# Optimization experiments

Hardware: AMD Instinct MI355X
Metric: run time of the kernel (lower is better)

Reference implementation:

```python
import jax, jax.numpy as jnp
import numpy as np

D = 128      # d_model
H = 8        # heads
HD = D // H  # head dim
FF = 1024    # feedforward
L = 6        # encoder layers
LN_EPS = 1e-5


def setup_inputs() -> dict:
    key = jax.random.key(0)
    ks = jax.random.split(key, 10)
    S, B = 512, 64
    p = lambda k, shape: jax.random.normal(k, shape, dtype=jnp.float32) * 0.02
    return {
        "src": jax.random.normal(ks[0], (S, B, D), dtype=jnp.float32),
        "Wqkv": p(ks[1], (L, 3 * D, D)), "bqkv": p(ks[2], (L, 3 * D)),
        "Wo": p(ks[3], (L, D, D)), "bo": p(ks[4], (L, D)),
        "ln1_g": jnp.ones((L, D), jnp.float32), "ln1_b": jnp.zeros((L, D), jnp.float32),
        "W1": p(ks[5], (L, FF, D)), "b1": p(ks[6], (L, FF)),
        "W2": p(ks[7], (L, D, FF)), "b2": p(ks[8], (L, D)),
        "ln2_g": jnp.ones((L, D), jnp.float32), "ln2_b": jnp.zeros((L, D), jnp.float32),
    }


def _layer_norm(x, g, b):
    mu = jnp.mean(x, axis=-1, keepdims=True)
    var = jnp.mean(jnp.square(x - mu), axis=-1, keepdims=True)
    return (x - mu) * jax.lax.rsqrt(var + LN_EPS) * g + b


def _pairwise_cos(x):
    # x: (B, S, D) -> clamped cosine similarity (B, S, S); single batched GEMM
    n = jnp.linalg.norm(x, axis=-1)                      # (B, S)
    sim = jnp.einsum('bid,bjd->bij', x, x) / (n[:, :, None] * n[:, None, :])
    return jnp.maximum(sim, 1e-6)


def _encoder_layer(x, Wqkv, bqkv, Wo, bo, g1, b1ln, W1, b1, W2, b2, g2, b2ln):
    # x: (B, S, D); PyTorch post-norm TransformerEncoderLayer (ReLU), eval mode (no dropout)
    B, S, _ = x.shape
    qkv = x @ Wqkv.T + bqkv                              # (B, S, 3D)
    q, k, v = jnp.split(qkv, 3, axis=-1)
    q = q.reshape(B, S, H, HD)
    k = k.reshape(B, S, H, HD)
    v = v.reshape(B, S, H, HD)
    scores = jnp.einsum('bqhd,bkhd->bhqk', q, k) / np.float32(np.sqrt(HD))
    attn = jax.nn.softmax(scores, axis=-1)
    o = jnp.einsum('bhqk,bkhd->bqhd', attn, v).reshape(B, S, D)
    o = o @ Wo.T + bo
    x = _layer_norm(x + o, g1, b1ln)
    ff = jax.nn.relu(x @ W1.T + b1) @ W2.T + b2
    return _layer_norm(x + ff, g2, b2ln)


def reference(src, Wqkv, bqkv, Wo, bo, ln1_g, ln1_b, W1, b1, W2, b2, ln2_g, ln2_b):
    x_bsd = jnp.transpose(src, (1, 0, 2))                # (B, S, D)
    cs = _pairwise_cos(x_bsd)
    h = x_bsd
    for i in range(L):
        h = _encoder_layer(h, Wqkv[i], bqkv[i], Wo[i], bo[i], ln1_g[i], ln1_b[i],
                           W1[i], b1[i], W2[i], b2[i], ln2_g[i], ln2_b[i])
    mask = jax.nn.sigmoid(h)
    out = mask * x_bsd
    out = out / jnp.maximum(jnp.linalg.norm(out, axis=-1, keepdims=True), 1e-12)
    sim = _pairwise_cos(out) + cs
    return jnp.clip(sim * 0.5, 0.1, 0.9)
```

## Files before the change

kernel.cpp:

```cpp
#include <hip/hip_runtime.h>
#include <cstdint>
#include <cstddef>

#define SS 512
#define BB 64
#define DD 128
#define HH 8
#define HDIM 16
#define FFD 1024
#define NL 6

typedef short bf16x8 __attribute__((ext_vector_type(8)));
typedef float f32x4 __attribute__((ext_vector_type(4)));

__device__ inline uint32_t pack2(float a, float b) {
  uint32_t r;
  asm("v_cvt_pk_bf16_f32 %0, %1, %2" : "=v"(r) : "v"(a), "v"(b));
  return r;
}

#define QSCALE 0.36067376022224085f

__global__ __launch_bounds__(256) void cvt_kernel(const float* __restrict__ s,
                                                  short* __restrict__ d, int n2) {
  int i = blockIdx.x * 256 + threadIdx.x;
  if (i < n2) {
    float2 v = ((const float2*)s)[i];
    ((uint32_t*)d)[i] = pack2(v.x, v.y);
  }
}

__global__ __launch_bounds__(256) void cvt_qkv_kernel(const float* __restrict__ s,
                                                      short* __restrict__ d) {
  int i = blockIdx.x * 256 + threadIdx.x;
  if (i < NL * 384 * 64) {
    const int within = i % (384 * 64);
    const float sc = (within < 128 * 64) ? QSCALE : 1.0f;
    float2 v = ((const float2*)s)[i];
    ((uint32_t*)d)[i] = pack2(v.x * sc, v.y * sc);
  }
}

__global__ __launch_bounds__(256) void scale_bq_kernel(const float* __restrict__ s,
                                                       float* __restrict__ d) {
  int i = blockIdx.x * 256 + threadIdx.x;
  if (i < NL * 384) {
    const float sc = ((i % 384) < 128) ? QSCALE : 1.0f;
    d[i] = s[i] * sc;
  }
}

__global__ __launch_bounds__(256) void transpose_rn_kernel(const float* __restrict__ src,
                                                           float* __restrict__ x0,
                                                           float* __restrict__ h,
                                                           short* __restrict__ hb,
                                                           short* __restrict__ xn) {
  const int wave = threadIdx.x >> 6;
  const int lane = threadIdx.x & 63;
  const int row = blockIdx.x * 4 + wave;
  const int b = row >> 9;
  const int s = row & 511;
  const float2 v = ((const float2*)(src + ((size_t)s * BB + b) * DD))[lane];
  ((float2*)(x0 + (size_t)row * DD))[lane] = v;
  ((float2*)(h + (size_t)row * DD))[lane] = v;
  ((uint32_t*)hb)[(size_t)row * 64 + lane] = pack2(v.x, v.y);
  float ss = v.x * v.x + v.y * v.y;
  #pragma unroll
  for (int off = 1; off < 64; off <<= 1) ss += __shfl_xor(ss, off);
  const float r = rsqrtf(ss);
  ((uint32_t*)xn)[(size_t)row * 64 + lane] = pack2(v.x * r, v.y * r);
}

template <int MODE, bool CBF, bool RELU, bool QPERM>
__global__ __launch_bounds__(256) void mgemm(const short* __restrict__ Ab0,
                                             const short* __restrict__ Bw,
                                             const float* __restrict__ bias,
                                             void* __restrict__ Cp,
                                             int M, int N, int K,
                                             long sA, long sB, long sC) {
  __shared__ uint32_t Xs[128 * 32];
  __shared__ uint32_t Wls[128 * 32];
  const int t = threadIdx.x;
  const int wave = t >> 6, lane = t & 63;
  const int g = lane >> 4, p = lane & 15;
  const int wr = wave >> 1, wc = wave & 1;
  const int m0 = blockIdx.y * 128, n0 = blockIdx.x * 128;
  const int z = blockIdx.z;
  const short* Ab = Ab0 + (size_t)z * sA;
  const short* Bb = Bw + (size_t)z * sB;
  float* Cf = (float*)Cp + (CBF ? (size_t)0 : (size_t)z * sC);
  short* Cb = (short*)Cp;

  f32x4 acc[4][4];
  #pragma unroll
  for (int i = 0; i < 4; ++i)
    #pragma unroll
    for (int j = 0; j < 4; ++j) acc[i][j] = (f32x4){0.f, 0.f, 0.f, 0.f};

  for (int kt = 0; kt < K; kt += 64) {
    __syncthreads();
    #pragma unroll
    for (int i = 0; i < 4; ++i) {
      const int idx = t + i * 256;
      const int row = idx >> 3, kc = idx & 7;
      const uint4 w = *(const uint4*)(Ab + (size_t)(m0 + row) * K + kt + kc * 8);
      *(uint4*)(Xs + row * 32 + ((kc ^ (row & 7)) << 2)) = w;
      const uint4 u = *(const uint4*)(Bb + (size_t)(n0 + row) * K + kt + kc * 8);
      *(uint4*)(Wls + row * 32 + ((kc ^ (row & 7)) << 2)) = u;
    }
    __syncthreads();
    #pragma unroll
    for (int kc32 = 0; kc32 < 2; ++kc32) {
      bf16x8 xf[4], wf[4];
      #pragma unroll
      for (int mi = 0; mi < 4; ++mi) {
        const int row = wr * 64 + mi * 16 + p;
        union { bf16x8 v; uint4 w; } u;
        u.w = *(const uint4*)(Xs + row * 32 + (((kc32 * 4 + g) ^ (row & 7)) << 2));
        xf[mi] = u.v;
      }
      #pragma unroll
      for (int ni = 0; ni < 4; ++ni) {
        const int row = wc * 64 + ni * 16 + p;
        union { bf16x8 v; uint4 w; } u;
        u.w = *(const uint4*)(Wls + row * 32 + (((kc32 * 4 + g) ^ (row & 7)) << 2));
        wf[ni] = u.v;
      }
      #pragma unroll
      for (int mi = 0; mi < 4; ++mi)
        #pragma unroll
        for (int ni = 0; ni < 4; ++ni)
          acc[mi][ni] = __builtin_amdgcn_mfma_f32_16x16x32_bf16(wf[ni], xf[mi], acc[mi][ni], 0, 0, 0);
    }
  }

  #pragma unroll
  for (int mi = 0; mi < 4; ++mi) {
    const int m = m0 + wr * 64 + mi * 16 + p;
    #pragma unroll
    for (int ni = 0; ni < 4; ++ni) {
      const int nb = n0 + wc * 64 + ni * 16 + g * 4;
      float c[4];
      if (MODE == 0) {
        const float4 bv = *(const float4*)(bias + nb);
        const float bp[4] = {bv.x, bv.y, bv.z, bv.w};
        #pragma unroll
        for (int r = 0; r < 4; ++r) {
          c[r] = acc[mi][ni][r] + bp[r];
          if (RELU) c[r] = fmaxf(c[r], 0.0f);
        }
      } else if (MODE == 1) {
        #pragma unroll
        for (int r = 0; r < 4; ++r) c[r] = fmaxf(acc[mi][ni][r], 1e-6f);
      } else {
        const float4 pv = *(const float4*)(Cf + (size_t)m * N + nb);
        const float pp[4] = {pv.x, pv.y, pv.z, pv.w};
        #pragma unroll
        for (int r = 0; r < 4; ++r) {
          float v = fmaxf(acc[mi][ni][r], 1e-6f);
          c[r] = fminf(fmaxf(0.5f * (v + pp[r]), 0.1f), 0.9f);
        }
      }
      if (QPERM) {
        const int bb2 = m >> 9, s = m & 511;
        const int which = nb >> 7, hh = (nb >> 4) & 7, d = nb & 15;
        uint2 w;
        w.x = pack2(c[0], c[1]);
        w.y = pack2(c[2], c[3]);
        *(uint2*)(Cb + ((((size_t)(bb2 * 3 + which) * 8 + hh) * 512 + s) * 16 + d)) = w;
      } else if (CBF) {
        uint2 w;
        w.x = pack2(c[0], c[1]);
        w.y = pack2(c[2], c[3]);
        *(uint2*)(Cb + (size_t)m * N + nb) = w;
      } else {
        float4 w;
        w.x = c[0]; w.y = c[1]; w.z = c[2]; w.w = c[3];
        *(float4*)(Cf + (size_t)m * N + nb) = w;
      }
    }
  }
}

__global__ __launch_bounds__(256) void wo_ffn_ln_kernel(const short* __restrict__ att,
                                                        const short* __restrict__ Wob,
                                                        const float* __restrict__ bov,
                                                        const float* __restrict__ lng1,
                                                        const float* __restrict__ lnb1,
                                                        const short* __restrict__ W1b,
                                                        const float* __restrict__ b1v,
                                                        const short* __restrict__ W2b,
                                                        const float* __restrict__ b2v,
                                                        const float* __restrict__ lng2,
                                                        const float* __restrict__ lnb2,
                                                        float* __restrict__ hx,
                                                        short* __restrict__ hb) {
  __shared__ uint32_t S[10240];
  uint32_t* WoLS = S;
  uint32_t* Tb   = S;
  uint32_t* W1base = S;
  uint32_t* W2base = S + 4096;
  const int t = threadIdx.x;
  const int w = t >> 6, lane = t & 63;
  const int g = lane >> 4, p = lane & 15;
  const int m0 = blockIdx.x * 64;
  const int m = m0 + w * 16 + p;
  const int lr = w * 16 + p;
  const int lkey = (lr & 3) | ((lr >> 1) & 12);

  bf16x8 af[4];
  #pragma unroll
  for (int kc = 0; kc < 4; ++kc) {
    union { bf16x8 v; uint4 u; } uu;
    uu.u = *(const uint4*)(att + (size_t)m * DD + kc * 32 + g * 8);
    af[kc] = uu.v;
  }
  #pragma unroll
  for (int i = 0; i < 8; ++i) {
    const int idx = i * 256 + t;
    const int row = idx >> 4, slot = idx & 15;
    const int key = (row & 3) | ((row >> 1) & 12);
    const uint4 u = *(const uint4*)(Wob + (size_t)row * DD + slot * 8);
    *(uint4*)(&WoLS[row * 64 + ((slot ^ key) << 2)]) = u;
  }
  __syncthreads();

  f32x4 acc[8];
  #pragma unroll
  for (int i = 0; i < 8; ++i) acc[i] = (f32x4){0.f, 0.f, 0.f, 0.f};
  #pragma unroll
  for (int kc = 0; kc < 4; ++kc) {
    #pragma unroll
    for (int ni = 0; ni < 8; ++ni) {
      const int row = ni * 16 + p;
      const int key = (row & 3) | ((row >> 1) & 12);
      union { bf16x8 v; uint4 u; } wf;
      wf.u = *(const uint4*)(&WoLS[row * 64 + (((kc * 4 + g) ^ key) << 2)]);
      acc[ni] = __builtin_amdgcn_mfma_f32_16x16x32_bf16(wf.v, af[kc], acc[ni], 0, 0, 0);
    }
  }

  float h1r[8][4];
  float s1r = 0.0f, s2r = 0.0f;
  #pragma unroll
  for (int ni = 0; ni < 8; ++ni) {
    const int nb = ni * 16 + g * 4;
    const float4 rv = *(const float4*)(hx + (size_t)m * DD + nb);
    const float4 bv = *(const float4*)(bov + nb);
    h1r[ni][0] = acc[ni][0] + bv.x + rv.x;
    h1r[ni][1] = acc[ni][1] + bv.y + rv.y;
    h1r[ni][2] = acc[ni][2] + bv.z + rv.z;
    h1r[ni][3] = acc[ni][3] + bv.w + rv.w;
    #pragma unroll
    for (int r = 0; r < 4; ++r) {
      s1r += h1r[ni][r];
      s2r += h1r[ni][r] * h1r[ni][r];
    }
  }
  s1r += __shfl_xor(s1r, 16); s1r += __shfl_xor(s1r, 32);
  s2r += __shfl_xor(s2r, 16); s2r += __shfl_xor(s2r, 32);
  {
    const float mu = s1r * (1.0f / 128.0f);
    const float rs = rsqrtf(fmaxf(s2r * (1.0f / 128.0f) - mu * mu, 0.0f) + 1e-5f);
    #pragma unroll
    for (int ni = 0; ni < 8; ++ni) {
      const int nb = ni * 16 + g * 4;
      const float4 gv = *(const float4*)(lng1 + nb);
      const float4 bv = *(const float4*)(lnb1 + nb);
      h1r[ni][0] = (h1r[ni][0] - mu) * rs * gv.x + bv.x;
      h1r[ni][1] = (h1r[ni][1] - mu) * rs * gv.y + bv.y;
      h1r[ni][2] = (h1r[ni][2] - mu) * rs * gv.z + bv.z;
      h1r[ni][3] = (h1r[ni][3] - mu) * rs * gv.w + bv.w;
    }
  }
  __syncthreads();

  #pragma unroll
  for (int ni = 0; ni < 8; ++ni) {
    const int w16 = ni * 8 + 2 * g;
    const int slot = w16 >> 2, offs = w16 & 3;
    uint2 pk;
    pk.x = pack2(h1r[ni][0], h1r[ni][1]);
    pk.y = pack2(h1r[ni][2], h1r[ni][3]);
    *(uint2*)(&Tb[lr * 64 + ((slot ^ lkey) << 2) + offs]) = pk;
  }
  __syncthreads();

  bf16x8 hsf[4];
  #pragma unroll
  for (int kc = 0; kc < 4; ++kc) {
    union { bf16x8 v; uint4 u; } uu;
    uu.u = *(const uint4*)(&Tb[lr * 64 + (((kc * 4 + g) ^ lkey) << 2)]);
    hsf[kc] = uu.v;
  }
  __syncthreads();

  uint4 rA0, rA1, rB0, rB1;

#define FFN_LOAD(c)                                                               \
  {                                                                               \
    const int nf0_ = (c) * 32;                                                    \
    rA0 = *(const uint4*)(W1b + (size_t)(nf0_ + (t >> 4)) * DD + (t & 15) * 8);   \
    rA1 = *(const uint4*)(W1b + (size_t)(nf0_ + 16 + (t >> 4)) * DD + (t & 15) * 8); \
    rB0 = *(const uint4*)(W2b + (size_t)(t >> 2) * FFD + nf0_ + (t & 3) * 8);     \
    rB1 = *(const uint4*)(W2b + (size_t)(64 + (t >> 2)) * FFD + nf0_ + (t & 3) * 8); \
  }

#define FFN_WRITE(bufA, bufB)                                                     \
  {                                                                               \
    uint32_t* W1p = W1base + (bufA) * 2048;                                       \
    uint32_t* W2p = W2base + (bufB) * 2048;                                       \
    const int rw0 = t >> 4, sl0 = t & 15;                                         \
    const int k0 = (rw0 & 3) | ((rw0 >> 1) & 12);                                 \
    *(uint4*)(&W1p[rw0 * 64 + ((sl0 ^ k0) << 2)]) = rA0;                          \
    const int rw1 = 16 + rw0;                                                     \
    const int k1 = (rw1 & 3) | ((rw1 >> 1) & 12);                                 \
    *(uint4*)(&W1p[rw1 * 64 + ((sl0 ^ k1) << 2)]) = rA1;                          \
    const int rw2 = t >> 2, sl2 = t & 3;                                          \
    *(uint4*)(&W2p[rw2 * 16 + ((sl2 ^ ((rw2 >> 1) & 3)) << 2)]) = rB0;            \
    const int rw3 = 64 + rw2;                                                     \
    *(uint4*)(&W2p[rw3 * 16 + ((sl2 ^ ((rw3 >> 1) & 3)) << 2)]) = rB1;            \
  }

  FFN_LOAD(0);
  FFN_WRITE(0, 0);
  __syncthreads();

  const int pr0 = 8 * (p >> 2) + (p & 3);
  const int pr1 = pr0 + 4;
  const int key0 = (pr0 & 3) | ((pr0 >> 1) & 12);
  const int key1 = (pr1 & 3) | ((pr1 >> 1) & 12);

  f32x4 acc2[8];
  #pragma unroll
  for (int i = 0; i < 8; ++i) acc2[i] = (f32x4){0.f, 0.f, 0.f, 0.f};
  const f32x4 zacc = {0.f, 0.f, 0.f, 0.f};

  bf16x8 pbv;
  int bPrev = 2, bCur = 0, bNext = 1;

  for (int c = 0; c < 32; ++c) {
    const int bA = c & 1;
    if (c + 1 < 32) FFN_LOAD(c + 1);

    const uint32_t* W1p = W1base + bA * 2048;
    f32x4 s0 = zacc, s1 = zacc;
    #pragma unroll
    for (int kc = 0; kc < 4; ++kc) {
      union { bf16x8 v; uint4 u; } a0, a1;
      a0.u = *(const uint4*)(&W1p[pr0 * 64 + (((kc * 4 + g) ^ key0) << 2)]);
      a1.u = *(const uint4*)(&W1p[pr1 * 64 + (((kc * 4 + g) ^ key1) << 2)]);
      s0 = __builtin_amdgcn_mfma_f32_16x16x32_bf16(a0.v, hsf[kc], s0, 0, 0, 0);
      s1 = __builtin_amdgcn_mfma_f32_16x16x32_bf16(a1.v, hsf[kc], s1, 0, 0, 0);
    }

    if (c > 0) {
      const uint32_t* W2p = W2base + bPrev * 2048;
      #pragma unroll
      for (int ni = 0; ni < 8; ++ni) {
        const int row = ni * 16 + p;
        union { bf16x8 v; uint4 u; } wf;
        wf.u = *(const uint4*)(&W2p[row * 16 + ((g ^ ((row >> 1) & 3)) << 2)]);
        acc2[ni] = __builtin_amdgcn_mfma_f32_16x16x32_bf16(wf.v, pbv, acc2[ni], 0, 0, 0);
      }
    }

    const int nf0 = c * 32;
    const float4 bb0 = *(const float4*)(b1v + nf0 + 8 * g);
    const float4 bb1 = *(const float4*)(b1v + nf0 + 8 * g + 4);
    union { bf16x8 v; uint4 u; } pb;
    pb.u.x = pack2(fmaxf(s0[0] + bb0.x, 0.0f), fmaxf(s0[1] + bb0.y, 0.0f));
    pb.u.y = pack2(fmaxf(s0[2] + bb0.z, 0.0f), fmaxf(s0[3] + bb0.w, 0.0f));
    pb.u.z = pack2(fmaxf(s1[0] + bb1.x, 0.0f), fmaxf(s1[1] + bb1.y, 0.0f));
    pb.u.w = pack2(fmaxf(s1[2] + bb1.z, 0.0f), fmaxf(s1[3] + bb1.w, 0.0f));
    pbv = pb.v;

    if (c + 1 < 32) FFN_WRITE(bA ^ 1, bNext);
    __syncthreads();

    bPrev = bCur; bCur = bNext; bNext = (bNext == 2) ? 0 : bNext + 1;
  }

  {
    const uint32_t* W2p = W2base + 1 * 2048;
    #pragma unroll
    for (int ni = 0; ni < 8; ++ni) {
      const int row = ni * 16 + p;
      union { bf16x8 v; uint4 u; } wf;
      wf.u = *(const uint4*)(&W2p[row * 16 + ((g ^ ((row >> 1) & 3)) << 2)]);
      acc2[ni] = __builtin_amdgcn_mfma_f32_16x16x32_bf16(wf.v, pbv, acc2[ni], 0, 0, 0);
    }
  }

  float t1 = 0.0f, t2 = 0.0f;
  #pragma unroll
  for (int ni = 0; ni < 8; ++ni) {
    const int nb = ni * 16 + g * 4;
    const float4 bv = *(const float4*)(b2v + nb);
    acc2[ni][0] += bv.x + h1r[ni][0];
    acc2[ni][1] += bv.y + h1r[ni][1];
    acc2[ni][2] += bv.z + h1r[ni][2];
    acc2[ni][3] += bv.w + h1r[ni][3];
    #pragma unroll
    for (int r = 0; r < 4; ++r) {
      t1 += acc2[ni][r];
      t2 += acc2[ni][r] * acc2[ni][r];
    }
  }
  t1 += __shfl_xor(t1, 16); t1 += __shfl_xor(t1, 32);
  t2 += __shfl_xor(t2, 16); t2 += __shfl_xor(t2, 32);
  const float mu2 = t1 * (1.0f / 128.0f);
  const float rs2 = rsqrtf(fmaxf(t2 * (1.0f / 128.0f) - mu2 * mu2, 0.0f) + 1e-5f);
  #pragma unroll
  for (int ni = 0; ni < 8; ++ni) {
    const int nb = ni * 16 + g * 4;
    const float4 gv = *(const float4*)(lng2 + nb);
    const float4 bv = *(const float4*)(lnb2 + nb);
    float c[4];
    c[0] = (acc2[ni][0] - mu2) * rs2 * gv.x + bv.x;
    c[1] = (acc2[ni][1] - mu2) * rs2 * gv.y + bv.y;
    c[2] = (acc2[ni][2] - mu2) * rs2 * gv.z + bv.z;
    c[3] = (acc2[ni][3] - mu2) * rs2 * gv.w + bv.w;
    float4 wv;
    wv.x = c[0]; wv.y = c[1]; wv.z = c[2]; wv.w = c[3];
    *(float4*)(hx + (size_t)m * DD + nb) = wv;
    uint2 wb;
    wb.x = pack2(c[0], c[1]);
    wb.y = pack2(c[2], c[3]);
    *(uint2*)(hb + (size_t)m * DD + nb) = wb;
  }
}

__global__ __launch_bounds__(512) void attn_mfma_kernel(const short* __restrict__ qkvp,
                                                        short* __restrict__ o_out) {
  const int h = blockIdx.x;
  const int b = blockIdx.y;
  const int z = blockIdx.z;
  const int t = threadIdx.x;
  const int wave = t >> 6;
  const int lane = t & 63;
  const int g = lane >> 4;
  const int p = lane & 15;

  __shared__ uint32_t Ks[512 * 8];
  __shared__ uint32_t Vs[16 * 256];

  const short* baseQ = qkvp + ((size_t)(b * 3 + 0) * 8 + h) * 8192;
  const short* baseK = qkvp + ((size_t)(b * 3 + 1) * 8 + h) * 8192;
  const short* baseV = qkvp + ((size_t)(b * 3 + 2) * 8 + h) * 8192;

  {
    const int row = t;
    const uint4 lo = *(const uint4*)(baseK + row * 16);
    const uint4 hi = *(const uint4*)(baseK + row * 16 + 8);
    const int f = ((row >> 3) & 1) << 2;
    *(uint4*)(Ks + row * 8 + f) = lo;
    *(uint4*)(Ks + row * 8 + (f ^ 4)) = hi;
  }
  {
    const int k = t;
    union { uint4 u[2]; short s[16]; } vv;
    vv.u[0] = *(const uint4*)(baseV + k * 16);
    vv.u[1] = *(const uint4*)(baseV + k * 16 + 8);
    const int wk = k >> 1;
    #pragma unroll
    for (int d = 0; d < 16; ++d) {
      const int word = d * 256 + (wk ^ ((d & 7) << 2));
      ((short*)(Vs + word))[k & 1] = vv.s[d];
    }
  }
  __syncthreads();

  const bf16x8 zfrag = {0, 0, 0, 0, 0, 0, 0, 0};
  const f32x4 zacc = {0.f, 0.f, 0.f, 0.f};

  #pragma unroll
  for (int qi = 0; qi < 2; ++qi) {
    const int qt = z * 16 + wave + qi * 8;
    bf16x8 qf = zfrag;
    if (g < 2) {
      union { bf16x8 v; uint4 w; } qu;
      qu.w = *(const uint4*)(baseQ + (qt * 16 + p) * 16 + g * 8);
      qf = qu.v;
    }

    f32x4 o = zacc;
    float lsum = 0.0f;

    for (int kv = 0; kv < 16; ++kv) {
      bf16x8 ka = zfrag, kb = zfrag;
      if (g < 2) {
        const int r0 = kv * 32 + 8 * (p >> 2) + (p & 3);
        const int r1 = r0 + 4;
        union { bf16x8 v; uint4 w; } u;
        u.w = *(const uint4*)(Ks + r0 * 8 + ((4 * g) ^ (((r0 >> 3) & 1) << 2)));
        ka = u.v;
        u.w = *(const uint4*)(Ks + r1 * 8 + ((4 * g) ^ (((r1 >> 3) & 1) << 2)));
        kb = u.v;
      }
      union { bf16x8 v; uint4 w; } vu;
      vu.w = *(const uint4*)(Vs + p * 256 + ((kv * 16 + g * 4) ^ ((p & 7) << 2)));

      const f32x4 s0 = __builtin_amdgcn_mfma_f32_16x16x32_bf16(ka, qf, zacc, 0, 0, 0);
      const f32x4 s1 = __builtin_amdgcn_mfma_f32_16x16x32_bf16(kb, qf, zacc, 0, 0, 0);

      float sv0[4], sv1[4];
      #pragma unroll
      for (int r = 0; r < 4; ++r) {
        sv0[r] = __builtin_amdgcn_exp2f(s0[r]);
        sv1[r] = __builtin_amdgcn_exp2f(s1[r]);
      }
      #pragma unroll
      for (int r = 0; r < 4; ++r) lsum += sv0[r] + sv1[r];

      union { bf16x8 v; uint4 w; } pu;
      pu.w.x = pack2(sv0[0], sv0[1]);
      pu.w.y = pack2(sv0[2], sv0[3]);
      pu.w.z = pack2(sv1[0], sv1[1]);
      pu.w.w = pack2(sv1[2], sv1[3]);

      o = __builtin_amdgcn_mfma_f32_16x16x32_bf16(pu.v, vu.v, o, 0, 0, 0);
    }

    lsum += __shfl_xor(lsum, 16);
    lsum += __shfl_xor(lsum, 32);
    const float li = 1.0f / lsum;
    #pragma unroll
    for (int r = 0; r < 4; ++r) {
      const float inv = __shfl(li, 4 * g + r);
      o_out[((size_t)(b * SS + qt * 16 + 4 * g + r)) * DD + h * HDIM + p] =
          (short)(pack2(o[r] * inv, 0.0f) & 0xffff);
    }
  }
}

__global__ __launch_bounds__(256) void mask_norm_kernel(const float* __restrict__ h,
                                                        const float* __restrict__ x0,
                                                        short* __restrict__ yn) {
  const int wave = threadIdx.x >> 6;
  const int lane = threadIdx.x & 63;
  const size_t row = (size_t)blockIdx.x * 4 + wave;
  const float2 hv = ((const float2*)(h + row * DD))[lane];
  const float2 xv = ((const float2*)(x0 + row * DD))[lane];
  const float a = xv.x / (1.0f + __expf(-hv.x));
  const float c = xv.y / (1.0f + __expf(-hv.y));
  float ss = a * a + c * c;
  #pragma unroll
  for (int off = 1; off < 64; off <<= 1) ss += __shfl_xor(ss, off);
  const float inv = 1.0f / fmaxf(sqrtf(ss), 1e-12f);
  ((uint32_t*)yn)[row * 64 + lane] = pack2(a * inv, c * inv);
}

extern "C" void kernel_launch(void* const* d_in, const int* in_sizes, int n_in,
                              void* d_out, int out_size, void* d_ws, size_t ws_size,
                              hipStream_t stream) {
  const float* src  = (const float*)d_in[0];
  const float* Wqkv = (const float*)d_in[1];
  const float* bqkv = (const float*)d_in[2];
  const float* Wo   = (const float*)d_in[3];
  const float* bo   = (const float*)d_in[4];
  const float* ln1g = (const float*)d_in[5];
  const float* ln1b = (const float*)d_in[6];
  const float* W1   = (const float*)d_in[7];
  const float* b1   = (const float*)d_in[8];
  const float* W2   = (const float*)d_in[9];
  const float* b2   = (const float*)d_in[10];
  const float* ln2g = (const float*)d_in[11];
  const float* ln2b = (const float*)d_in[12];
  float* out = (float*)d_out;

  char* W = (char*)d_ws;
  const size_t MB = 1048576;
  float* x0  = (float*)(W);
  float* h   = (float*)(W + 16 * MB);
  short* hb  = (short*)(W + 32 * MB);
  short* qkvp = (short*)(W + 40 * MB);
  short* att = (short*)(W + 128 * MB);
  short* xn  = (short*)(W + 136 * MB);
  short* yn  = (short*)(W + 144 * MB);
  short* wqB = (short*)(W + 152 * MB);
  short* woB = wqB + (size_t)NL * 384 * DD;
  short* w1B = woB + (size_t)NL * DD * DD;
  short* w2B = w1B + (size_t)NL * FFD * DD;
  float* bq2 = (float*)(w2B + (size_t)NL * DD * FFD);

  const dim3 blk(256);
  const int ROWS = BB * SS;

  cvt_qkv_kernel<<<(NL * 384 * 64 + 255) / 256, blk, 0, stream>>>(Wqkv, wqB);
  cvt_kernel<<<(NL * DD * DD / 2 + 255) / 256, blk, 0, stream>>>(Wo, woB, NL * DD * DD / 2);
  cvt_kernel<<<(NL * FFD * DD / 2 + 255) / 256, blk, 0, stream>>>(W1, w1B, NL * FFD * DD / 2);
  cvt_kernel<<<(NL * DD * FFD / 2 + 255) / 256, blk, 0, stream>>>(W2, w2B, NL * DD * FFD / 2);
  scale_bq_kernel<<<(NL * 384 + 255) / 256, blk, 0, stream>>>(bqkv, bq2);

  transpose_rn_kernel<<<ROWS / 4, blk, 0, stream>>>(src, x0, h, hb, xn);
  mgemm<1, false, false, false><<<dim3(4, 4, BB), blk, 0, stream>>>(
      xn, xn, nullptr, out, SS, SS, DD, (long)SS * DD, (long)SS * DD, (long)SS * SS);

  for (int l = 0; l < NL; ++l) {
    mgemm<0, true, false, true><<<dim3(3, ROWS / 128, 1), blk, 0, stream>>>(
        hb, wqB + (size_t)l * 384 * DD, bq2 + l * 384, qkvp, ROWS, 384, DD, 0, 0, 0);
    attn_mfma_kernel<<<dim3(HH, BB, 2), dim3(512), 0, stream>>>(qkvp, att);
    wo_ffn_ln_kernel<<<dim3(ROWS / 64), blk, 0, stream>>>(
        att, woB + (size_t)l * DD * DD, bo + l * DD, ln1g + l * DD, ln1b + l * DD,
        w1B + (size_t)l * FFD * DD, b1 + l * FFD,
        w2B + (size_t)l * DD * FFD, b2 + l * DD,
        ln2g + l * DD, ln2b + l * DD, h, hb);
  }

  mask_norm_kernel<<<ROWS / 4, blk, 0, stream>>>(h, x0, yn);
  mgemm<2, false, false, false><<<dim3(4, 4, BB), blk, 0, stream>>>(
      yn, yn, nullptr, out, SS, SS, DD, (long)SS * DD, (long)SS * DD, (long)SS * SS);
}
```

Before: 544.1 us.

## Fuse both pairwise cosine GEMMs into one kernel, drop intermediate fp32 write

```diff
diff --git a/kernel.cpp b/kernel.cpp
--- a/kernel.cpp
+++ b/kernel.cpp
@@ -71,13 +71,10 @@
   ((uint32_t*)xn)[(size_t)row * 64 + lane] = pack2(v.x * r, v.y * r);
 }
 
-template <int MODE, bool CBF, bool RELU, bool QPERM>
-__global__ __launch_bounds__(256) void mgemm(const short* __restrict__ Ab0,
-                                             const short* __restrict__ Bw,
-                                             const float* __restrict__ bias,
-                                             void* __restrict__ Cp,
-                                             int M, int N, int K,
-                                             long sA, long sB, long sC) {
+__global__ __launch_bounds__(256) void mgemm_qkv(const short* __restrict__ Ab,
+                                                 const short* __restrict__ Bw,
+                                                 const float* __restrict__ bias,
+                                                 short* __restrict__ Cb) {
   __shared__ uint32_t Xs[128 * 32];
   __shared__ uint32_t Wls[128 * 32];
   const int t = threadIdx.x;
@@ -85,11 +82,7 @@
   const int g = lane >> 4, p = lane & 15;
   const int wr = wave >> 1, wc = wave & 1;
   const int m0 = blockIdx.y * 128, n0 = blockIdx.x * 128;
-  const int z = blockIdx.z;
-  const short* Ab = Ab0 + (size_t)z * sA;
-  const short* Bb = Bw + (size_t)z * sB;
-  float* Cf = (float*)Cp + (CBF ? (size_t)0 : (size_t)z * sC);
-  short* Cb = (short*)Cp;
+  const int K = DD, N = 384;
 
   f32x4 acc[4][4];
   #pragma unroll
@@ -105,7 +98,7 @@
       const int row = idx >> 3, kc = idx & 7;
       const uint4 w = *(const uint4*)(Ab + (size_t)(m0 + row) * K + kt + kc * 8);
       *(uint4*)(Xs + row * 32 + ((kc ^ (row & 7)) << 2)) = w;
-      const uint4 u = *(const uint4*)(Bb + (size_t)(n0 + row) * K + kt + kc * 8);
+      const uint4 u = *(const uint4*)(Bw + (size_t)(n0 + row) * K + kt + kc * 8);
       *(uint4*)(Wls + row * 32 + ((kc ^ (row & 7)) << 2)) = u;
     }
     __syncthreads();
@@ -140,45 +133,116 @@
     #pragma unroll
     for (int ni = 0; ni < 4; ++ni) {
       const int nb = n0 + wc * 64 + ni * 16 + g * 4;
+      const float4 bv = *(const float4*)(bias + nb);
       float c[4];
-      if (MODE == 0) {
-        const float4 bv = *(const float4*)(bias + nb);
-        const float bp[4] = {bv.x, bv.y, bv.z, bv.w};
-        #pragma unroll
-        for (int r = 0; r < 4; ++r) {
-          c[r] = acc[mi][ni][r] + bp[r];
-          if (RELU) c[r] = fmaxf(c[r], 0.0f);
-        }
-      } else if (MODE == 1) {
-        #pragma unroll
-        for (int r = 0; r < 4; ++r) c[r] = fmaxf(acc[mi][ni][r], 1e-6f);
-      } else {
-        const float4 pv = *(const float4*)(Cf + (size_t)m * N + nb);
-        const float pp[4] = {pv.x, pv.y, pv.z, pv.w};
-        #pragma unroll
-        for (int r = 0; r < 4; ++r) {
-          float v = fmaxf(acc[mi][ni][r], 1e-6f);
-          c[r] = fminf(fmaxf(0.5f * (v + pp[r]), 0.1f), 0.9f);
-        }
-      }
-      if (QPERM) {
-        const int bb2 = m >> 9, s = m & 511;
-        const int which = nb >> 7, hh = (nb >> 4) & 7, d = nb & 15;
-        uint2 w;
-        w.x = pack2(c[0], c[1]);
-        w.y = pack2(c[2], c[3]);
-        *(uint2*)(Cb + ((((size_t)(bb2 * 3 + which) * 8 + hh) * 512 + s) * 16 + d)) = w;
-      } else if (CBF) {
-        uint2 w;
-        w.x = pack2(c[0], c[1]);
-        w.y = pack2(c[2], c[3]);
-        *(uint2*)(Cb + (size_t)m * N + nb) = w;
-      } else {
-        float4 w;
-        w.x = c[0]; w.y = c[1]; w.z = c[2]; w.w = c[3];
-        *(float4*)(Cf + (size_t)m * N + nb) = w;
-      }
-    }
+      c[0] = acc[mi][ni][0] + bv.x;
+      c[1] = acc[mi][ni][1] + bv.y;
+      c[2] = acc[mi][ni][2] + bv.z;
+      c[3] = acc[mi][ni][3] + bv.w;
+      const int bb2 = m >> 9, s = m & 511;
+      const int which = nb >> 7, hh = (nb >> 4) & 7, d = nb & 15;
+      uint2 w;
+      w.x = pack2(c[0], c[1]);
+      w.y = pack2(c[2], c[3]);
+      *(uint2*)(Cb + ((((size_t)(bb2 * 3 + which) * 8 + hh) * 512 + s) * 16 + d)) = w;
+    }
+  }
+}
+
+__global__ __launch_bounds__(256) void cos2_kernel(const short* __restrict__ xn,
+                                                   const short* __restrict__ yn,
+                                                   float* __restrict__ out) {
+  __shared__ uint32_t Js[128 * 64];
+  const int t = threadIdx.x;
+  const int w = t >> 6, lane = t & 63;
+  const int g = lane >> 4, p = lane & 15;
+  const int j0 = blockIdx.x * 128;
+  const int i0 = blockIdx.y * 64;
+  const int b = blockIdx.z;
+  const short* xb = xn + (size_t)b * SS * DD;
+  const short* yb = yn + (size_t)b * SS * DD;
+  const int i = i0 + w * 16 + p;
+
+  bf16x8 af[4];
+  #pragma unroll
+  for (int kc = 0; kc < 4; ++kc) {
+    union { bf16x8 v; uint4 u; } uu;
+    uu.u = *(const uint4*)(xb + (size_t)i * DD + kc * 32 + g * 8);
+    af[kc] = uu.v;
+  }
+  #pragma unroll
+  for (int q = 0; q < 8; ++q) {
+    const int idx = q * 256 + t;
+    const int row = idx >> 4, slot = idx & 15;
+    const int key = (row & 3) | ((row >> 1) & 12);
+    const uint4 u = *(const uint4*)(xb + (size_t)(j0 + row) * DD + slot * 8);
+    *(uint4*)(&Js[row * 64 + ((slot ^ key) << 2)]) = u;
+  }
+  __syncthreads();
+
+  f32x4 acc[8];
+  #pragma unroll
+  for (int q = 0; q < 8; ++q) acc[q] = (f32x4){0.f, 0.f, 0.f, 0.f};
+  #pragma unroll
+  for (int kc = 0; kc < 4; ++kc) {
+    #pragma unroll
+    for (int ni = 0; ni < 8; ++ni) {
+      const int row = ni * 16 + p;
+      const int key = (row & 3) | ((row >> 1) & 12);
+      union { bf16x8 v; uint4 u; } jf;
+      jf.u = *(const uint4*)(&Js[row * 64 + (((kc * 4 + g) ^ key) << 2)]);
+      acc[ni] = __builtin_amdgcn_mfma_f32_16x16x32_bf16(jf.v, af[kc], acc[ni], 0, 0, 0);
+    }
+  }
+  float prev[8][4];
+  #pragma unroll
+  for (int ni = 0; ni < 8; ++ni)
+    #pragma unroll
+    for (int r = 0; r < 4; ++r) prev[ni][r] = fmaxf(acc[ni][r], 1e-6f);
+  __syncthreads();
+
+  #pragma unroll
+  for (int kc = 0; kc < 4; ++kc) {
+    union { bf16x8 v; uint4 u; } uu;
+    uu.u = *(const uint4*)(yb + (size_t)i * DD + kc * 32 + g * 8);
+    af[kc] = uu.v;
+  }
+  #pragma unroll
+  for (int q = 0; q < 8; ++q) {
+    const int idx = q * 256 + t;
+    const int row = idx >> 4, slot = idx & 15;
+    const int key = (row & 3) | ((row >> 1) & 12);
+    const uint4 u = *(const uint4*)(yb + (size_t)(j0 + row) * DD + slot * 8);
+    *(uint4*)(&Js[row * 64 + ((slot ^ key) << 2)]) = u;
+  }
+  __syncthreads();
+
+  #pragma unroll
+  for (int q = 0; q < 8; ++q) acc[q] = (f32x4){0.f, 0.f, 0.f, 0.f};
+  #pragma unroll
+  for (int kc = 0; kc < 4; ++kc) {
+    #pragma unroll
+    for (int ni = 0; ni < 8; ++ni) {
+      const int row = ni * 16 + p;
+      const int key = (row & 3) | ((row >> 1) & 12);
+      union { bf16x8 v; uint4 u; } jf;
+      jf.u = *(const uint4*)(&Js[row * 64 + (((kc * 4 + g) ^ key) << 2)]);
+      acc[ni] = __builtin_amdgcn_mfma_f32_16x16x32_bf16(jf.v, af[kc], acc[ni], 0, 0, 0);
+    }
+  }
+
+  float* ob = out + (size_t)b * SS * SS;
+  #pragma unroll
+  for (int ni = 0; ni < 8; ++ni) {
+    const int j = j0 + ni * 16 + g * 4;
+    float4 wv;
+    float* pw = &wv.x;
+    #pragma unroll
+    for (int r = 0; r < 4; ++r) {
+      const float v = fmaxf(acc[ni][r], 1e-6f);
+      pw[r] = fminf(fmaxf(0.5f * (v + prev[ni][r]), 0.1f), 0.9f);
+    }
+    *(float4*)(ob + (size_t)i * SS + j) = wv;
   }
 }
 
@@ -594,12 +658,10 @@
   scale_bq_kernel<<<(NL * 384 + 255) / 256, blk, 0, stream>>>(bqkv, bq2);
 
   transpose_rn_kernel<<<ROWS / 4, blk, 0, stream>>>(src, x0, h, hb, xn);
-  mgemm<1, false, false, false><<<dim3(4, 4, BB), blk, 0, stream>>>(
-      xn, xn, nullptr, out, SS, SS, DD, (long)SS * DD, (long)SS * DD, (long)SS * SS);
 
   for (int l = 0; l < NL; ++l) {
-    mgemm<0, true, false, true><<<dim3(3, ROWS / 128, 1), blk, 0, stream>>>(
-        hb, wqB + (size_t)l * 384 * DD, bq2 + l * 384, qkvp, ROWS, 384, DD, 0, 0, 0);
+    mgemm_qkv<<<dim3(3, ROWS / 128), blk, 0, stream>>>(
+        hb, wqB + (size_t)l * 384 * DD, bq2 + l * 384, qkvp);
     attn_mfma_kernel<<<dim3(HH, BB, 2), dim3(512), 0, stream>>>(qkvp, att);
     wo_ffn_ln_kernel<<<dim3(ROWS / 64), blk, 0, stream>>>(
         att, woB + (size_t)l * DD * DD, bo + l * DD, ln1g + l * DD, ln1b + l * DD,
@@ -609,6 +671,5 @@
   }
 
   mask_norm_kernel<<<ROWS / 4, blk, 0, stream>>>(h, x0, yn);
-  mgemm<2, false, false, false><<<dim3(4, 4, BB), blk, 0, stream>>>(
-      yn, yn, nullptr, out, SS, SS, DD, (long)SS * DD, (long)SS * DD, (long)SS * SS);
-}
+  cos2_kernel<<<dim3(4, 8, BB), blk, 0, stream>>>(xn, yn, out);
+}
```

Measured after the change: 532.7 us. 2.1% less time.
